# Optimization experiments

Hardware: AMD Instinct MI355X
Metric: run time of the kernel (lower is better)

## Reference

```python
import math
import jax, jax.numpy as jnp
import numpy as np

B, S, D, H, DK = 2, 2048, 1024, 16, 64
NUM_BUCKETS, MAX_DISTANCE = 32, 128


def _relative_position_bucket(rel_pos):
    # bidirectional=True (encoder): is_decoder=False
    nb = NUM_BUCKETS // 2
    rel_buckets = (rel_pos > 0).astype(jnp.int32) * nb
    rp = jnp.abs(rel_pos)
    max_exact = nb // 2
    is_small = rp < max_exact
    rp_large = max_exact + (
        jnp.log(rp.astype(jnp.float32) / max_exact)
        / math.log(MAX_DISTANCE / max_exact)
        * (nb - max_exact)
    ).astype(jnp.int32)
    rp_large = jnp.minimum(rp_large, nb - 1)
    return rel_buckets + jnp.where(is_small, rp, rp_large)


def compute_bias(rel_bias, q_len, k_len):
    ctx = jnp.arange(q_len, dtype=jnp.int32)[:, None]
    mem = jnp.arange(k_len, dtype=jnp.int32)[None, :]
    buckets = _relative_position_bucket(mem - ctx)          # [q,k]
    vals = rel_bias[buckets]                                 # [q,k,H]
    return jnp.transpose(vals, (2, 0, 1))[None]              # [1,H,q,k]


def setup_inputs() -> dict:
    key = jax.random.key(0)
    ks = jax.random.split(key, 6)
    scale = 0.02
    return {
        "hidden_states": jax.random.normal(ks[0], (B, S, D), jnp.float32),
        "Wq": jax.random.normal(ks[1], (D, H * DK), jnp.float32) * scale,
        "Wk": jax.random.normal(ks[2], (D, H * DK), jnp.float32) * scale,
        "Wv": jax.random.normal(ks[3], (D, H * DK), jnp.float32) * scale,
        "Wo": jax.random.normal(ks[4], (H * DK, D), jnp.float32) * scale,
        "rel_bias": jax.random.normal(ks[5], (NUM_BUCKETS, H), jnp.float32) * scale,
    }


def reference(hidden_states, Wq, Wk, Wv, Wo, rel_bias):
    b, s, _ = hidden_states.shape

    def shape(x):  # [b,s,H*DK] -> [b,H,s,DK]
        return x.reshape(b, s, H, DK).transpose(0, 2, 1, 3)

    q = shape(hidden_states @ Wq)
    k = shape(hidden_states @ Wk)
    v = shape(hidden_states @ Wv)

    # T5: no 1/sqrt(d_k) scaling
    scores = jnp.einsum("bhqd,bhkd->bhqk", q, k)
    position_bias = compute_bias(rel_bias, s, s)             # [1,H,s,s]
    scores = scores + position_bias
    attn = jax.nn.softmax(scores.astype(jnp.float32), axis=-1).astype(scores.dtype)
    out = jnp.einsum("bhqk,bhkd->bhqd", attn, v)
    out = out.transpose(0, 2, 1, 3).reshape(b, s, H * DK)
    return out @ Wo
```

## Files before the change

### kernel.cpp

```cpp
#include <hip/hip_runtime.h>

#define HH 16
#define DKK 64
#define SS 2048
#define BB 2
#define DD 1024

typedef __attribute__((ext_vector_type(4))) float f32x4;
typedef __attribute__((ext_vector_type(16))) float f32x16;
typedef __attribute__((ext_vector_type(8))) short bf16x8;
typedef __attribute__((ext_vector_type(4))) short s16x4;
typedef __attribute__((ext_vector_type(4))) int i32x4;

#define WAITCNT_VM0 0xF70

__device__ __forceinline__ short bf16b(float f) {
    union { float f; unsigned u; } x; x.f = f;
    unsigned r = (x.u + 0x7fffu + ((x.u >> 16) & 1u)) >> 16;
    return (short)r;
}

__device__ __forceinline__ f32x4 mfma16(bf16x8 a, bf16x8 b, f32x4 c) {
    return __builtin_amdgcn_mfma_f32_16x16x32_bf16(a, b, c, 0, 0, 0);
}

__device__ __forceinline__ f32x16 mfma32(bf16x8 a, bf16x8 b, f32x16 c) {
    return __builtin_amdgcn_mfma_f32_32x32x16_bf16(a, b, c, 0, 0, 0);
}

__device__ __forceinline__ void lds16(const short* g, short* l) {
    __builtin_amdgcn_global_load_lds(
        (const __attribute__((address_space(1))) void*)g,
        (__attribute__((address_space(3))) void*)l, 16, 0, 0);
}

__device__ __forceinline__ int cvtpk(float lo, float hi) {
    int r;
    asm("v_cvt_pk_bf16_f32 %0, %1, %2" : "=v"(r) : "v"(lo), "v"(hi));
    return r;
}

__device__ __forceinline__ void swap32(int& a, int& b) {
    asm("v_permlane32_swap_b32 %0, %1" : "+v"(a), "+v"(b));
}

__global__ __launch_bounds__(256) void prep(
    const float* __restrict__ hs,
    const float* __restrict__ W0, const float* __restrict__ W1,
    const float* __restrict__ W2, const float* __restrict__ W3,
    const float* __restrict__ rb,
    short* __restrict__ hsb,
    short* __restrict__ T0, short* __restrict__ T1,
    short* __restrict__ T2, short* __restrict__ T3,
    float* __restrict__ tab) {
    __shared__ short tile[32][33];
    int blk = blockIdx.x, tid = threadIdx.x;
    if (blk < 4096) {
        int i = (blk * 256 + tid) * 4;
        f32x4 v = *(const f32x4*)(hs + i);
        s16x4 o;
        o.x = bf16b(v.x); o.y = bf16b(v.y); o.z = bf16b(v.z); o.w = bf16b(v.w);
        *(s16x4*)(hsb + i) = o;
    } else if (blk < 8192) {
        int t = blk - 4096;
        int z = t >> 10, r = t & 1023;
        int bx = r & 31, by = r >> 5;
        const float* W; short* T;
        switch (z) {
            case 0: W = W0; T = T0; break;
            case 1: W = W1; T = T1; break;
            case 2: W = W2; T = T2; break;
            default: W = W3; T = T3; break;
        }
        int n0 = bx * 32, k0 = by * 32;
        int tx = tid & 31, ty = (tid >> 5) * 4;
#pragma unroll
        for (int i = 0; i < 4; i++)
            tile[ty + i][tx] = bf16b(W[(k0 + ty + i) * DD + n0 + tx]);
        __syncthreads();
#pragma unroll
        for (int i = 0; i < 4; i++)
            T[(n0 + ty + i) * DD + k0 + tx] = tile[tx][ty + i];
    } else {
        int idx = (blk - 8192) * 256 + tid;
        if (idx < HH * 4095) {
            int h = idx / 4095, d = idx % 4095;
            int rel = d - 2047;
            int bucket = (rel > 0) ? 16 : 0;
            unsigned rr = (rel < 0) ? (unsigned)(-rel) : (unsigned)rel;
            int add;
            if (rr < 8) add = (int)rr;
            else {
                int e = 31 - __clz(rr);
                unsigned long long r2 = (unsigned long long)rr * (unsigned long long)rr;
                int f = 2 * e + ((r2 >= (2ull << (2 * e))) ? 1 : 0);
                add = 8 + (f - 6);
                if (add > 15) add = 15;
            }
            bucket += add;
            tab[h * 4095 + d] = rb[bucket * HH + h] * 1.44269504f;
        }
    }
}

__global__ __launch_bounds__(256) void gemm_qkv(
    const short* __restrict__ A, const short* __restrict__ Wt,
    short* __restrict__ Cq, short* __restrict__ Ck, short* __restrict__ Cvt) {
    const int K = 1024;
    __shared__ short As[128 * 32];
    __shared__ short Bs[128 * 32];
    int tid = threadIdx.x;
    int wave = tid >> 6, lane = tid & 63;
    int quad = lane >> 4, l16 = lane & 15;
    int m0 = blockIdx.y * 128, n0 = blockIdx.x * 128;

    int wm = (wave & 1) * 64, wn = (wave >> 1) * 64;
    int r0 = tid >> 2, c0 = (tid & 3) * 8;

    f32x4 acc[4][4];
#pragma unroll
    for (int i = 0; i < 4; i++)
#pragma unroll
        for (int j = 0; j < 4; j++) acc[i][j] = (f32x4){0.f, 0.f, 0.f, 0.f};

    for (int k0 = 0; k0 < K; k0 += 32) {
        __syncthreads();
        lds16(A + (size_t)(m0 + r0) * K + k0 + c0, As + wave * 512);
        lds16(A + (size_t)(m0 + 64 + r0) * K + k0 + c0, As + 2048 + wave * 512);
        lds16(Wt + (size_t)(n0 + r0) * K + k0 + c0, Bs + wave * 512);
        lds16(Wt + (size_t)(n0 + 64 + r0) * K + k0 + c0, Bs + 2048 + wave * 512);
        __syncthreads();
        bf16x8 af[4], bfr[4];
#pragma unroll
        for (int t = 0; t < 4; t++) {
            af[t] = *(const bf16x8*)(As + (wm + t * 16 + l16) * 32 + quad * 8);
            bfr[t] = *(const bf16x8*)(Bs + (wn + t * 16 + l16) * 32 + quad * 8);
        }
#pragma unroll
        for (int mt = 0; mt < 4; mt++)
#pragma unroll
            for (int nt = 0; nt < 4; nt++)
                acc[mt][nt] = mfma16(af[mt], bfr[nt], acc[mt][nt]);
    }

#pragma unroll
    for (int mt = 0; mt < 4; mt++) {
#pragma unroll
        for (int nt = 0; nt < 4; nt++) {
#pragma unroll
            for (int r = 0; r < 4; r++) {
                int gm = m0 + wm + mt * 16 + quad * 4 + r;
                int gn = n0 + wn + nt * 16 + l16;
                int b = gm >> 11, s = gm & 2047;
                int which = gn >> 10;
                int h = (gn >> 6) & 15, dk = gn & 63;
                short bv = bf16b(acc[mt][nt][r]);
                if (which == 0)
                    Cq[(((size_t)(b * HH + h)) * SS + s) * DKK + dk] = bv;
                else if (which == 1)
                    Ck[(((size_t)(b * HH + h)) * SS + s) * DKK + dk] = bv;
                else
                    Cvt[(((size_t)(b * HH + h)) * DKK + dk) * SS + s] = bv;
            }
        }
    }
}

__global__ __launch_bounds__(256) void gemm_out(
    const short* __restrict__ A, const short* __restrict__ Wt,
    float* __restrict__ Cout) {
    const int K = 1024, N = 1024;
    __shared__ short As[64 * 32];
    __shared__ short Bs[128 * 32];
    int tid = threadIdx.x;
    int wave = tid >> 6, lane = tid & 63;
    int quad = lane >> 4, l16 = lane & 15;
    int m0 = blockIdx.y * 64, n0 = blockIdx.x * 128;

    int wm = (wave & 1) * 32, wn = (wave >> 1) * 64;
    int r0 = tid >> 2, c0 = (tid & 3) * 8;

    f32x4 acc[2][4];
#pragma unroll
    for (int i = 0; i < 2; i++)
#pragma unroll
        for (int j = 0; j < 4; j++) acc[i][j] = (f32x4){0.f, 0.f, 0.f, 0.f};

    for (int k0 = 0; k0 < K; k0 += 32) {
        __syncthreads();
        lds16(A + (size_t)(m0 + r0) * K + k0 + c0, As + wave * 512);
        lds16(Wt + (size_t)(n0 + r0) * K + k0 + c0, Bs + wave * 512);
        lds16(Wt + (size_t)(n0 + 64 + r0) * K + k0 + c0, Bs + 2048 + wave * 512);
        __syncthreads();
        bf16x8 af[2], bfr[4];
#pragma unroll
        for (int t = 0; t < 2; t++)
            af[t] = *(const bf16x8*)(As + (wm + t * 16 + l16) * 32 + quad * 8);
#pragma unroll
        for (int t = 0; t < 4; t++)
            bfr[t] = *(const bf16x8*)(Bs + (wn + t * 16 + l16) * 32 + quad * 8);
#pragma unroll
        for (int mt = 0; mt < 2; mt++)
#pragma unroll
            for (int nt = 0; nt < 4; nt++)
                acc[mt][nt] = mfma16(af[mt], bfr[nt], acc[mt][nt]);
    }

#pragma unroll
    for (int mt = 0; mt < 2; mt++)
#pragma unroll
        for (int nt = 0; nt < 4; nt++)
#pragma unroll
            for (int r = 0; r < 4; r++) {
                int gm = m0 + wm + mt * 16 + quad * 4 + r;
                int gn = n0 + wn + nt * 16 + l16;
                Cout[(size_t)gm * N + gn] = acc[mt][nt][r];
            }
}

__global__ __launch_bounds__(256, 1) void attn(
    const short* __restrict__ Q, const short* __restrict__ Kmat,
    const short* __restrict__ Vt, const float* __restrict__ btab,
    short* __restrict__ O) {
    __shared__ short Ks[2][64 * 64];
    __shared__ short Vs[2][64 * 64];
    __shared__ float Linv[4][64];

    int tid = threadIdx.x;
    int wave = tid >> 6, lane = tid & 63;
    int el = lane & 31, hi = lane >> 5;
    int ex7 = el & 7;
    int bh = blockIdx.x;
    int h = bh & 15, b = bh >> 4;
    int q0b = blockIdx.y * 256;
    int q0w = q0b + wave * 64;

    const short* Qb = Q + (size_t)bh * SS * DKK;
    const short* Kb = Kmat + (size_t)bh * SS * DKK;
    const short* Vb = Vt + (size_t)bh * DKK * SS;
    const float* bt = btab + h * 4095;

    float blo = bt[2047 - 128];
    float bhi = bt[2047 + 128];

    int kro = tid >> 3;
    int gk = (tid & 7) ^ (kro & 7);
    const short* Kg0 = Kb + (size_t)kro * DKK + gk * 8;
    const short* Kg1 = Kb + (size_t)(kro + 32) * DKK + gk * 8;
    const short* Vg0 = Vb + (size_t)kro * SS + gk * 8;
    const short* Vg1 = Vb + (size_t)(kro + 32) * SS + gk * 8;

    bf16x8 qB[2][4];
#pragma unroll
    for (int qt = 0; qt < 2; qt++)
#pragma unroll
        for (int c = 0; c < 4; c++)
            qB[qt][c] = *(const bf16x8*)(
                Qb + (size_t)(q0w + qt * 32 + el) * DKK + c * 16 + hi * 8);

    f32x16 o[2][2];
#pragma unroll
    for (int qt = 0; qt < 2; qt++)
#pragma unroll
        for (int m = 0; m < 2; m++)
#pragma unroll
            for (int i = 0; i < 16; i++) o[qt][m][i] = 0.f;
    float ls[2][4];
#pragma unroll
    for (int qt = 0; qt < 2; qt++)
#pragma unroll
        for (int i = 0; i < 4; i++) ls[qt][i] = 0.f;

    int bq[2] = {2047 - q0w - el, 2047 - (q0w + 32) - el};

    lds16(Kg0, &Ks[0][wave * 512]);
    lds16(Kg1, &Ks[0][2048 + wave * 512]);
    lds16(Vg0, &Vs[0][wave * 512]);
    lds16(Vg1, &Vs[0][2048 + wave * 512]);

    int cur = 0;
    for (int kc = 0; kc < SS; kc += 64) {
        __syncthreads();
        int kn = (kc + 64) & (SS - 1);
        int nxt = cur ^ 1;
        lds16(Kg0 + (size_t)kn * DKK, &Ks[nxt][wave * 512]);
        lds16(Kg1 + (size_t)kn * DKK, &Ks[nxt][2048 + wave * 512]);
        lds16(Vg0 + kn, &Vs[nxt][wave * 512]);
        lds16(Vg1 + kn, &Vs[nxt][2048 + wave * 512]);

        const short* Ksc = &Ks[cur][0];
        const short* Vsc = &Vs[cur][0];

        bf16x8 vf[4][2];
#pragma unroll
        for (int c4 = 0; c4 < 4; c4++)
#pragma unroll
            for (int m = 0; m < 2; m++)
                vf[c4][m] = *(const bf16x8*)(
                    Vsc + (m * 32 + el) * 64 + (((2 * c4 + hi) ^ ex7) * 8));

#pragma unroll
        for (int st = 0; st < 2; st++) {
            bf16x8 kA[4];
#pragma unroll
            for (int c = 0; c < 4; c++)
                kA[c] = *(const bf16x8*)(
                    Ksc + (st * 32 + el) * 64 + (((2 * c + hi) ^ ex7) * 8));
            int ks = kc + st * 32;

#pragma unroll
            for (int qt = 0; qt < 2; qt++) {
                int q0 = q0w + qt * 32;
                f32x16 acc;
#pragma unroll
                for (int i = 0; i < 16; i++) acc[i] = 0.f;
                __builtin_amdgcn_s_setprio(1);
#pragma unroll
                for (int c = 0; c < 4; c++)
                    acc = mfma32(kA[c], qB[qt][c], acc);
                __builtin_amdgcn_s_setprio(0);

                float br[16];
                if (ks > q0 - 159 && ks < q0 + 159) {
#pragma unroll
                    for (int r = 0; r < 16; r++)
                        br[r] = bt[bq[qt] + ks + ((r & 3) + 8 * (r >> 2) + 4 * hi)];
                } else {
                    float bc = (ks <= q0 - 159) ? blo : bhi;
#pragma unroll
                    for (int r = 0; r < 16; r++) br[r] = bc;
                }

                float p[16];
#pragma unroll
                for (int r = 0; r < 16; r++)
                    p[r] = __builtin_amdgcn_exp2f(
                        fmaf(acc[r], 1.44269504f, br[r]));
#pragma unroll
                for (int r = 0; r < 16; r += 4) {
                    ls[qt][0] += p[r];     ls[qt][1] += p[r + 1];
                    ls[qt][2] += p[r + 2]; ls[qt][3] += p[r + 3];
                }

                int A1 = cvtpk(p[0], p[1]),   A2 = cvtpk(p[2], p[3]);
                int B1 = cvtpk(p[4], p[5]),   B2 = cvtpk(p[6], p[7]);
                int C1 = cvtpk(p[8], p[9]),   C2 = cvtpk(p[10], p[11]);
                int D1 = cvtpk(p[12], p[13]), D2 = cvtpk(p[14], p[15]);
                swap32(A1, B1); swap32(A2, B2);
                swap32(C1, D1); swap32(C2, D2);
                bf16x8 pf0 = __builtin_bit_cast(bf16x8, (i32x4){A1, A2, B1, B2});
                bf16x8 pf1 = __builtin_bit_cast(bf16x8, (i32x4){C1, C2, D1, D2});

                __builtin_amdgcn_s_setprio(1);
                o[qt][0] = mfma32(pf0, vf[st * 2 + 0][0], o[qt][0]);
                o[qt][1] = mfma32(pf0, vf[st * 2 + 0][1], o[qt][1]);
                o[qt][0] = mfma32(pf1, vf[st * 2 + 1][0], o[qt][0]);
                o[qt][1] = mfma32(pf1, vf[st * 2 + 1][1], o[qt][1]);
                __builtin_amdgcn_s_setprio(0);
            }
        }
        cur ^= 1;
    }
    __builtin_amdgcn_s_waitcnt(WAITCNT_VM0);

#pragma unroll
    for (int qt = 0; qt < 2; qt++) {
        float lsum = (ls[qt][0] + ls[qt][1]) + (ls[qt][2] + ls[qt][3]);
        float tot = lsum + __shfl_xor(lsum, 32);
        float inv = 1.f / tot;
        if (hi == 0) Linv[wave][qt * 32 + el] = inv;
    }
    __asm__ __volatile__("" ::: "memory");

#pragma unroll
    for (int qt = 0; qt < 2; qt++)
#pragma unroll
        for (int r = 0; r < 16; r++) {
            int qm = (r & 3) + 8 * (r >> 2) + 4 * hi;
            float iv = Linv[wave][qt * 32 + qm];
            size_t base =
                ((size_t)(b * SS + q0w + qt * 32 + qm)) * (HH * DKK) + h * DKK;
            O[base + el] = bf16b(o[qt][0][r] * iv);
            O[base + 32 + el] = bf16b(o[qt][1][r] * iv);
        }
}

extern "C" void kernel_launch(void* const* d_in, const int* in_sizes, int n_in,
                              void* d_out, int out_size, void* d_ws, size_t ws_size,
                              hipStream_t stream) {
    const float* hs = (const float*)d_in[0];
    const float* Wq = (const float*)d_in[1];
    const float* Wk = (const float*)d_in[2];
    const float* Wv = (const float*)d_in[3];
    const float* Wo = (const float*)d_in[4];
    const float* rb = (const float*)d_in[5];
    float* out = (float*)d_out;

    char* ws = (char*)d_ws;
    size_t off = 0;
    auto alloc = [&](size_t bytes) -> void* {
        void* p = (void*)(ws + off);
        off += (bytes + 255) & ~(size_t)255;
        return p;
    };
    const size_t M = (size_t)BB * SS;
    short* hsb = (short*)alloc(M * DD * 2);
    short* WqT = (short*)alloc((size_t)DD * DD * 2);
    short* WkT = (short*)alloc((size_t)DD * DD * 2);
    short* WvT = (short*)alloc((size_t)DD * DD * 2);
    short* WoT = (short*)alloc((size_t)DD * DD * 2);
    short* Qb  = (short*)alloc(M * DD * 2);
    short* Kb  = (short*)alloc(M * DD * 2);
    short* VTb = (short*)alloc(M * DD * 2);
    short* Ab  = (short*)alloc(M * DD * 2);
    float* btab = (float*)alloc((size_t)HH * 4095 * 4);

    prep<<<8448, 256, 0, stream>>>(hs, Wq, Wk, Wv, Wo, rb,
                                   hsb, WqT, WkT, WvT, WoT, btab);
    gemm_qkv<<<dim3(24, 32), 256, 0, stream>>>(hsb, WqT, Qb, Kb, VTb);
    attn<<<dim3(32, 8), 256, 0, stream>>>(Qb, Kb, VTb, btab, Ab);
    gemm_out<<<dim3(8, 64), 256, 0, stream>>>(Ab, WoT, out);
}
```

Baseline: 212.6 us.

## Split attention key range across wave pairs and double the grid

Each block now covers 128 queries instead of 256. Two wave pairs each process half of the key sequence into separate LDS buffers, and their partial outputs and row sums are combined through shared memory at the end. The grid doubles and launch bounds allow two blocks per CU. The aim is better CU utilisation and latency hiding, at the cost of twice the LDS footprint, a cross-wave reduction epilogue, and Q being reloaded in more blocks.

Result: faster. 194.3 us (-8.6%).

```diff
diff --git a/kernel.cpp b/kernel.cpp
--- a/kernel.cpp
+++ b/kernel.cpp
@@ -218,22 +218,24 @@
             }
 }
 
-__global__ __launch_bounds__(256, 1) void attn(
+__global__ __launch_bounds__(256, 2) void attn(
     const short* __restrict__ Q, const short* __restrict__ Kmat,
     const short* __restrict__ Vt, const float* __restrict__ btab,
     short* __restrict__ O) {
-    __shared__ short Ks[2][64 * 64];
-    __shared__ short Vs[2][64 * 64];
-    __shared__ float Linv[4][64];
+    __shared__ short Ks[2][2][64 * 64];
+    __shared__ short Vs[2][2][64 * 64];
+    __shared__ float Ls[2][256];
 
     int tid = threadIdx.x;
     int wave = tid >> 6, lane = tid & 63;
+    int qw = wave & 1, half = wave >> 1;
     int el = lane & 31, hi = lane >> 5;
     int ex7 = el & 7;
     int bh = blockIdx.x;
     int h = bh & 15, b = bh >> 4;
-    int q0b = blockIdx.y * 256;
-    int q0w = q0b + wave * 64;
+    int q0b = blockIdx.y * 128;
+    int q0w = q0b + qw * 64;
+    int ko = half * 1024;
 
     const short* Qb = Q + (size_t)bh * SS * DKK;
     const short* Kb = Kmat + (size_t)bh * SS * DKK;
@@ -243,12 +245,22 @@
     float blo = bt[2047 - 128];
     float bhi = bt[2047 + 128];
 
-    int kro = tid >> 3;
-    int gk = (tid & 7) ^ (kro & 7);
-    const short* Kg0 = Kb + (size_t)kro * DKK + gk * 8;
-    const short* Kg1 = Kb + (size_t)(kro + 32) * DKK + gk * 8;
-    const short* Vg0 = Vb + (size_t)kro * SS + gk * 8;
-    const short* Vg1 = Vb + (size_t)(kro + 32) * SS + gk * 8;
+    int tid_h = tid & 127;
+    int wh = tid_h >> 6;
+    int kro = tid_h >> 3;
+    int gk = (tid_h & 7) ^ (kro & 7);
+    const short* Kg = Kb + (size_t)(ko + kro) * DKK + gk * 8;
+    const short* Vg = Vb + (size_t)kro * SS + ko + gk * 8;
+
+    auto stage = [&](int buf, int kofs) {
+#pragma unroll
+        for (int j = 0; j < 4; j++) {
+            lds16(Kg + (size_t)(kofs + j * 16) * DKK,
+                  &Ks[half][buf][j * 1024 + wh * 512]);
+            lds16(Vg + kofs + (size_t)(j * 16) * SS,
+                  &Vs[half][buf][j * 1024 + wh * 512]);
+        }
+    };
 
     bf16x8 qB[2][4];
 #pragma unroll
@@ -273,23 +285,16 @@
 
     int bq[2] = {2047 - q0w - el, 2047 - (q0w + 32) - el};
 
-    lds16(Kg0, &Ks[0][wave * 512]);
-    lds16(Kg1, &Ks[0][2048 + wave * 512]);
-    lds16(Vg0, &Vs[0][wave * 512]);
-    lds16(Vg1, &Vs[0][2048 + wave * 512]);
+    stage(0, 0);
 
     int cur = 0;
-    for (int kc = 0; kc < SS; kc += 64) {
-        __syncthreads();
-        int kn = (kc + 64) & (SS - 1);
-        int nxt = cur ^ 1;
-        lds16(Kg0 + (size_t)kn * DKK, &Ks[nxt][wave * 512]);
-        lds16(Kg1 + (size_t)kn * DKK, &Ks[nxt][2048 + wave * 512]);
-        lds16(Vg0 + kn, &Vs[nxt][wave * 512]);
-        lds16(Vg1 + kn, &Vs[nxt][2048 + wave * 512]);
-
-        const short* Ksc = &Ks[cur][0];
-        const short* Vsc = &Vs[cur][0];
+    for (int kc2 = 0; kc2 < 1024; kc2 += 64) {
+        __syncthreads();
+        int kn2 = (kc2 + 64) & 1023;
+        stage(cur ^ 1, kn2);
+
+        const short* Ksc = &Ks[half][cur][0];
+        const short* Vsc = &Vs[half][cur][0];
 
         bf16x8 vf[4][2];
 #pragma unroll
@@ -306,7 +311,7 @@
             for (int c = 0; c < 4; c++)
                 kA[c] = *(const bf16x8*)(
                     Ksc + (st * 32 + el) * 64 + (((2 * c + hi) ^ ex7) * 8));
-            int ks = kc + st * 32;
+            int ks = ko + kc2 + st * 32;
 
 #pragma unroll
             for (int qt = 0; qt < 2; qt++) {
@@ -363,26 +368,56 @@
     }
     __builtin_amdgcn_s_waitcnt(WAITCNT_VM0);
 
+    float toth[2];
 #pragma unroll
     for (int qt = 0; qt < 2; qt++) {
         float lsum = (ls[qt][0] + ls[qt][1]) + (ls[qt][2] + ls[qt][3]);
-        float tot = lsum + __shfl_xor(lsum, 32);
-        float inv = 1.f / tot;
-        if (hi == 0) Linv[wave][qt * 32 + el] = inv;
-    }
-    __asm__ __volatile__("" ::: "memory");
-
-#pragma unroll
-    for (int qt = 0; qt < 2; qt++)
+        toth[qt] = lsum + __shfl_xor(lsum, 32);
+    }
+
+    __syncthreads();
+
+    float* Ob0 = (float*)&Ks[0][0][0];
+    float* Ob1 = (float*)&Vs[0][0][0];
+    int obase = (qw * 64 + lane) * 32;
+
+    if (half == 1) {
+        if (hi == 0) {
+            Ls[0][qw * 32 + el] = toth[0];
+            Ls[1][qw * 32 + el] = toth[1];
+        }
+#pragma unroll
+        for (int j = 0; j < 16; j++) {
+            Ob0[obase + (j ^ el)] = o[0][0][j];
+            Ob0[obase + ((16 + j) ^ el)] = o[0][1][j];
+            Ob1[obase + (j ^ el)] = o[1][0][j];
+            Ob1[obase + ((16 + j) ^ el)] = o[1][1][j];
+        }
+    }
+    __syncthreads();
+    if (half == 0) {
+#pragma unroll
+        for (int qt = 0; qt < 2; qt++) {
+            float tot = toth[qt] + Ls[qt][qw * 32 + el];
+            if (hi == 0) Ls[qt][128 + qw * 32 + el] = 1.f / tot;
+        }
+        __asm__ __volatile__("" ::: "memory");
 #pragma unroll
         for (int r = 0; r < 16; r++) {
             int qm = (r & 3) + 8 * (r >> 2) + 4 * hi;
-            float iv = Linv[wave][qt * 32 + qm];
-            size_t base =
-                ((size_t)(b * SS + q0w + qt * 32 + qm)) * (HH * DKK) + h * DKK;
-            O[base + el] = bf16b(o[qt][0][r] * iv);
-            O[base + 32 + el] = bf16b(o[qt][1][r] * iv);
-        }
+#pragma unroll
+            for (int qt = 0; qt < 2; qt++) {
+                float iv = Ls[qt][128 + qw * 32 + qm];
+                const float* Obx = qt ? Ob1 : Ob0;
+                float a0 = o[qt][0][r] + Obx[obase + (r ^ el)];
+                float a1 = o[qt][1][r] + Obx[obase + ((16 + r) ^ el)];
+                size_t base =
+                    ((size_t)(b * SS + q0w + qt * 32 + qm)) * (HH * DKK) + h * DKK;
+                O[base + el] = bf16b(a0 * iv);
+                O[base + 32 + el] = bf16b(a1 * iv);
+            }
+        }
+    }
 }
 
 extern "C" void kernel_launch(void* const* d_in, const int* in_sizes, int n_in,
@@ -418,6 +453,6 @@
     prep<<<8448, 256, 0, stream>>>(hs, Wq, Wk, Wv, Wo, rb,
                                    hsb, WqT, WkT, WvT, WoT, btab);
     gemm_qkv<<<dim3(24, 32), 256, 0, stream>>>(hsb, WqT, Qb, Kb, VTb);
-    attn<<<dim3(32, 8), 256, 0, stream>>>(Qb, Kb, VTb, btab, Ab);
+    attn<<<dim3(32, 16), 256, 0, stream>>>(Qb, Kb, VTb, btab, Ab);
     gemm_out<<<dim3(8, 64), 256, 0, stream>>>(Ab, WoT, out);
 }
```
